# Kernel tuning notes

Measured on AMD Instinct MI355X. Metric: run time of the kernel, lower is better.

## Reference

```python
import jax, jax.numpy as jnp
import numpy as np

# ---- static config ----
B, D, H, W, C = 4, 8, 56, 56, 192
Md, Mh, Mw = 2, 7, 7
Sd, Sh, Sw = 1, 3, 3
NH = 6
HD = C // NH
SCALE = HD ** -0.5
N = Md * Mh * Mw  # 98
NW = (D // Md) * (H // Mh) * (W // Mw)  # 256 windows per batch element


def _rel_pos_index():
    coords = np.stack(np.meshgrid(np.arange(Md), np.arange(Mh), np.arange(Mw), indexing='ij'))
    cf = coords.reshape(3, -1)
    rc = (cf[:, :, None] - cf[:, None, :]).transpose(1, 2, 0)
    rc[..., 0] += Md - 1
    rc[..., 1] += Mh - 1
    rc[..., 2] += Mw - 1
    rc[..., 0] *= (2 * Mh - 1) * (2 * Mw - 1)
    rc[..., 1] *= 2 * Mw - 1
    return rc.sum(-1)  # (N, N) int

REL_IDX = jnp.asarray(_rel_pos_index())


def _build_attn_mask():
    img = np.zeros((D, H, W), dtype=np.float32)
    cnt = 0
    for ds in (slice(0, -Md), slice(-Md, -Sd), slice(-Sd, None)):
        for hs in (slice(0, -Mh), slice(-Mh, -Sh), slice(-Sh, None)):
            for ws in (slice(0, -Mw), slice(-Mw, -Sw), slice(-Sw, None)):
                img[ds, hs, ws] = cnt
                cnt += 1
    mw = img.reshape(D // Md, Md, H // Mh, Mh, W // Mw, Mw)
    mw = mw.transpose(0, 2, 4, 1, 3, 5).reshape(-1, N)  # (NW, N)
    am = mw[:, None, :] - mw[:, :, None]
    return np.where(am != 0, -100.0, 0.0).astype(np.float32)  # (NW, N, N)


def window_partition(x):  # (B, D, H, W, C) -> (B*NW, N, C)
    x = x.reshape(B, D // Md, Md, H // Mh, Mh, W // Mw, Mw, C)
    return x.transpose(0, 1, 3, 5, 2, 4, 6, 7).reshape(-1, N, C)


def window_reverse(w):  # (B*NW, N, C) -> (B, D, H, W, C)
    x = w.reshape(B, D // Md, H // Mh, W // Mw, Md, Mh, Mw, C)
    return x.transpose(0, 1, 4, 2, 5, 3, 6, 7).reshape(B, D, H, W, C)


def layer_norm(x, g, b, eps=1e-5):
    mu = x.mean(-1, keepdims=True)
    var = ((x - mu) ** 2).mean(-1, keepdims=True)
    return (x - mu) * jax.lax.rsqrt(var + eps) * g + b


def setup_inputs() -> dict:
    key = jax.random.key(0)
    ks = jax.random.split(key, 6)
    return {
        'x': jax.random.normal(ks[0], (B, D * H * W, C), jnp.float32),
        'attn_mask': jnp.asarray(_build_attn_mask()),
        'norm1_g': jnp.ones((C,), jnp.float32),
        'norm1_b': jnp.zeros((C,), jnp.float32),
        'qkv_w': jax.random.normal(ks[1], (3 * C, C), jnp.float32) * 0.02,
        'qkv_b': jnp.zeros((3 * C,), jnp.float32),
        'rel_bias': jax.random.normal(ks[2], ((2 * Md - 1) * (2 * Mh - 1) * (2 * Mw - 1), NH), jnp.float32) * 0.02,
        'proj_w': jax.random.normal(ks[3], (C, C), jnp.float32) * 0.02,
        'proj_b': jnp.zeros((C,), jnp.float32),
        'fc1_w': jax.random.normal(ks[4], (C, C), jnp.float32) * 0.02,
        'fc1_b': jnp.zeros((C,), jnp.float32),
    }


def reference(x, attn_mask, norm1_g, norm1_b, qkv_w, qkv_b, rel_bias, proj_w, proj_b, fc1_w, fc1_b):
    shortcut = x
    h = layer_norm(x, norm1_g, norm1_b).reshape(B, D, H, W, C)
    # cyclic shift (dims divisible by window -> no padding needed)
    h = jnp.roll(h, shift=(-Sd, -Sh, -Sw), axis=(1, 2, 3))
    xw = window_partition(h)  # (B*NW, N, C)
    B_ = xw.shape[0]
    qkv = (xw @ qkv_w.T + qkv_b).reshape(B_, N, 3, NH, HD).transpose(2, 0, 3, 1, 4)
    q, k, v = qkv[0], qkv[1], qkv[2]  # (B_, NH, N, HD)
    attn = jnp.einsum('bhnd,bhmd->bhnm', q * SCALE, k)
    bias = rel_bias[REL_IDX.reshape(-1)].reshape(N, N, NH).transpose(2, 0, 1)  # (NH, N, N)
    attn = attn + bias[None]
    # additive shift mask per window
    attn = attn.reshape(B, NW, NH, N, N) + attn_mask[None, :, None]
    attn = jax.nn.softmax(attn.reshape(B_, NH, N, N), axis=-1)
    out = jnp.einsum('bhnm,bhmd->bhnd', attn, v).transpose(0, 2, 1, 3).reshape(B_, N, C)
    out = out @ proj_w.T + proj_b
    h = window_reverse(out)
    h = jnp.roll(h, shift=(Sd, Sh, Sw), axis=(1, 2, 3)).reshape(B, D * H * W, C)
    h = jax.nn.gelu(h @ fc1_w.T + fc1_b, approximate=False)
    return shortcut + h
```

## Files before the change

### kernel.cpp

```cpp
#include <hip/hip_runtime.h>
#include <cstdint>
#include <cstddef>

typedef __bf16 bf16_t;
typedef __bf16 bf16x8 __attribute__((ext_vector_type(8)));
typedef float  f32x4  __attribute__((ext_vector_type(4)));

#define DHW   25088
#define SCALE 0.17677669529663687f

__device__ inline f32x4 mfma16(bf16x8 a, bf16x8 b, f32x4 c) {
  return __builtin_amdgcn_mfma_f32_16x16x32_bf16(a, b, c, 0, 0, 0);
}

__global__ __launch_bounds__(256) void prep_kernel(
    const float* __restrict__ qkv_w, const float* __restrict__ proj_w,
    const float* __restrict__ fc1_w,
    bf16_t* __restrict__ wq, bf16_t* __restrict__ wp, bf16_t* __restrict__ wf)
{
  int idx = blockIdx.x * 256 + threadIdx.x;
  if (idx < 110592) { wq[idx] = (bf16_t)qkv_w[idx]; return; }
  idx -= 110592;
  if (idx < 36864) { wp[idx] = (bf16_t)proj_w[idx]; return; }
  idx -= 36864;
  if (idx < 36864) { wf[idx] = (bf16_t)fc1_w[idx]; }
}

__global__ __launch_bounds__(256) void prep_bm_kernel(
    const float* __restrict__ rel_bias, const float* __restrict__ mask,
    bf16_t* __restrict__ bmr)
{
  int idx = blockIdx.x * 256 + threadIdx.x;
  int e    = idx & 31;
  int lane = (idx >> 5) & 63;
  int t    = idx >> 11;
  int mt   = t % 7;
  int wh   = t / 7;
  int winb = wh / 6, h = wh - winb * 6;
  int g = lane >> 4, li = lane & 15;
  int nt2 = e >> 2, v = e & 3;
  int row = mt * 16 + g * 4 + v;
  int col = nt2 * 16 + li;
  float val = -1e30f;
  if (row < 98 && col < 98 && nt2 < 7) {
    int di = row / 49 - col / 49 + 1;
    int hi = (row / 7) % 7 - (col / 7) % 7 + 6;
    int wi = row % 7 - col % 7 + 6;
    int rid = di * 169 + hi * 13 + wi;
    val = mask[winb * 9604 + row * 98 + col] + rel_bias[rid * 6 + h];
  }
  bmr[idx] = (bf16_t)val;
}

__global__ __launch_bounds__(256) void ln_kernel(
    const float* __restrict__ x, const float* __restrict__ gw,
    const float* __restrict__ bw_, bf16_t* __restrict__ xn)
{
  int orow = blockIdx.x * 4 + (threadIdx.x >> 6);
  int lane = threadIdx.x & 63;
  int win = orow / 98, tok = orow % 98;
  int b = win >> 8, wr = win & 255;
  int bd = wr >> 6, bh = (wr >> 3) & 7, bwi = wr & 7;
  int md = tok / 49, mh = (tok / 7) % 7, mw = tok % 7;
  int d = (bd * 2 + md + 1) & 7;
  int h = bh * 7 + mh + 3; if (h >= 56) h -= 56;
  int w = bwi * 7 + mw + 3; if (w >= 56) w -= 56;
  const float* xr = x + ((size_t)b * DHW + (size_t)((d * 56 + h) * 56 + w)) * 192;
  float v0 = xr[lane], v1 = xr[lane + 64], v2 = xr[lane + 128];
  float s = v0 + v1 + v2, sq = v0 * v0 + v1 * v1 + v2 * v2;
  #pragma unroll
  for (int off = 1; off < 64; off <<= 1) {
    s  += __shfl_xor(s,  off, 64);
    sq += __shfl_xor(sq, off, 64);
  }
  float mu = s * (1.0f / 192.0f);
  float var = sq * (1.0f / 192.0f) - mu * mu;
  float rstd = rsqrtf(var + 1e-5f);
  bf16_t* o = xn + (size_t)orow * 192;
  o[lane]       = (bf16_t)((v0 - mu) * rstd * gw[lane]       + bw_[lane]);
  o[lane + 64]  = (bf16_t)((v1 - mu) * rstd * gw[lane + 64]  + bw_[lane + 64]);
  o[lane + 128] = (bf16_t)((v2 - mu) * rstd * gw[lane + 128] + bw_[lane + 128]);
}

template<int MODE>
__global__ __launch_bounds__(256) void gemm_kernel(
    const bf16_t* __restrict__ A, const bf16_t* __restrict__ W,
    const float* __restrict__ bias, int ntiles, int ncols,
    bf16_t* __restrict__ outb, float* __restrict__ outf,
    const float* __restrict__ resid)
{
  __shared__ __align__(16) bf16_t As[64][200];
  __shared__ __align__(16) bf16_t Bs[64][200];
  int tid = threadIdx.x;
  int nt = blockIdx.x % ntiles, mt = blockIdx.x / ntiles;
  int row0 = mt * 64, n0 = nt * 64;
  #pragma unroll
  for (int i = 0; i < 6; i++) {
    int c = tid + 256 * i;
    int r = c / 24, ck = c % 24;
    *(uint4*)&As[r][ck * 8] = *(const uint4*)(A + (size_t)(row0 + r) * 192 + ck * 8);
    *(uint4*)&Bs[r][ck * 8] = *(const uint4*)(W + (size_t)(n0 + r) * 192 + ck * 8);
  }
  __syncthreads();
  int wid = tid >> 6, lane = tid & 63;
  int wm = wid >> 1, wn = wid & 1;
  int g = lane >> 4, li = lane & 15;
  f32x4 acc[2][2] = {};
  #pragma unroll
  for (int ks = 0; ks < 6; ks++) {
    int ko = ks * 32 + g * 8;
    bf16x8 a0 = *(const bf16x8*)&As[wm * 32 + li][ko];
    bf16x8 a1 = *(const bf16x8*)&As[wm * 32 + 16 + li][ko];
    bf16x8 b0 = *(const bf16x8*)&Bs[wn * 32 + li][ko];
    bf16x8 b1 = *(const bf16x8*)&Bs[wn * 32 + 16 + li][ko];
    acc[0][0] = mfma16(a0, b0, acc[0][0]);
    acc[0][1] = mfma16(a0, b1, acc[0][1]);
    acc[1][0] = mfma16(a1, b0, acc[1][0]);
    acc[1][1] = mfma16(a1, b1, acc[1][1]);
  }
  #pragma unroll
  for (int mi = 0; mi < 2; mi++)
  #pragma unroll
  for (int ni = 0; ni < 2; ni++)
  #pragma unroll
  for (int v = 0; v < 4; v++) {
    int row = row0 + wm * 32 + mi * 16 + g * 4 + v;
    int col = n0 + wn * 32 + ni * 16 + li;
    float val = acc[mi][ni][v] + bias[col];
    if (MODE == 0) {
      outb[(size_t)row * ncols + col] = (bf16_t)val;
    } else if (MODE == 1) {
      int win = row / 98, tok = row % 98;
      int b = win >> 8, wr = win & 255;
      int bd = wr >> 6, bh = (wr >> 3) & 7, bwi = wr & 7;
      int md = tok / 49, mh = (tok / 7) % 7, mw = tok % 7;
      int d = (bd * 2 + md + 1) & 7;
      int hh = bh * 7 + mh + 3; if (hh >= 56) hh -= 56;
      int w2 = bwi * 7 + mw + 3; if (w2 >= 56) w2 -= 56;
      size_t grow = (size_t)b * DHW + (size_t)((d * 56 + hh) * 56 + w2);
      outb[grow * 192 + col] = (bf16_t)val;
    } else {
      float ge = 0.5f * val * (1.0f + erff(val * 0.70710678118654752f));
      size_t o = (size_t)row * 192 + col;
      outf[o] = resid[o] + ge;
    }
  }
}

__global__ __launch_bounds__(448, 6) void attn_kernel(
    const bf16_t* __restrict__ qkv, const bf16_t* __restrict__ bmr,
    bf16_t* __restrict__ ao)
{
  __shared__ __align__(16) bf16_t U[15232];
  __shared__ __align__(16) bf16_t Vt[32][136];
  int bid = blockIdx.x;
  int h = bid % 6, win = bid / 6;
  int winb = win & 255;
  int tid = threadIdx.x;
  int wid = tid >> 6, lane = tid & 63;
  int mt = wid, g = lane >> 4, li = lane & 15;

  const bf16_t* bmp = bmr + ((((size_t)(winb * 6 + h)) * 7 + mt) * 64 + lane) * 32;
  bf16x8 bm0 = *(const bf16x8*)(bmp);
  bf16x8 bm1 = *(const bf16x8*)(bmp + 8);
  bf16x8 bm2 = *(const bf16x8*)(bmp + 16);
  bf16x8 bm3 = *(const bf16x8*)(bmp + 24);

  const bf16_t* base = qkv + (size_t)win * 98 * 576 + h * 32;
  #define QS(r, c) U[(r) * 40 + (c)]
  #define KS(r, c) U[4480 + (r) * 40 + (c)]
  #define PS(r, c) U[(r) * 136 + (c)]
  for (int c = tid; c < 784; c += 448) {
    int cc = c < 392 ? c : c - 392;
    int tok = cc >> 2, part = cc & 3;
    uint4 u = *(const uint4*)(base + (c < 392 ? 0 : 192) + tok * 576 + part * 8);
    if (c < 392) *(uint4*)&QS(tok, part * 8) = u;
    else         *(uint4*)&KS(tok, part * 8) = u;
  }
  if (tid < 112) {
    uint4 z = {0, 0, 0, 0};
    int a = tid >> 6;
    int r = 98 + ((tid & 63) >> 2), part = tid & 3;
    if (r < 112) {
      if (a == 0) *(uint4*)&QS(r, part * 8) = z;
      else        *(uint4*)&KS(r, part * 8) = z;
    }
  }
  if (tid < 392) {
    int tok = tid >> 2, part = tid & 3;
    bf16x8 u = *(const bf16x8*)(base + 384 + tok * 576 + part * 8);
    #pragma unroll
    for (int j = 0; j < 8; j++) Vt[part * 8 + j][tok] = u[j];
  }
  for (int e2 = tid; e2 < 960; e2 += 448) {
    int r = e2 / 30, ci = 98 + e2 % 30;
    Vt[r][ci] = (bf16_t)0.0f;
  }
  __syncthreads();

  bf16x8 af = *(const bf16x8*)&QS(mt * 16 + li, g * 8);
  float logit[7][4];
  #pragma unroll
  for (int nt2 = 0; nt2 < 7; nt2++) {
    bf16x8 bfr = *(const bf16x8*)&KS(nt2 * 16 + li, g * 8);
    f32x4 z = {};
    f32x4 S = mfma16(af, bfr, z);
    #pragma unroll
    for (int v = 0; v < 4; v++) {
      int e = nt2 * 4 + v;
      float bmv = (e < 8) ? (float)bm0[e] : (e < 16) ? (float)bm1[e - 8]
                : (e < 24) ? (float)bm2[e - 16] : (float)bm3[e - 24];
      logit[nt2][v] = S[v] * SCALE + bmv;
    }
  }
  __syncthreads();

  #pragma unroll
  for (int v = 0; v < 4; v++) {
    float mx = logit[0][v];
    #pragma unroll
    for (int nt2 = 1; nt2 < 7; nt2++) mx = fmaxf(mx, logit[nt2][v]);
    #pragma unroll
    for (int off = 1; off < 16; off <<= 1) mx = fmaxf(mx, __shfl_xor(mx, off, 64));
    float se = 0.f;
    #pragma unroll
    for (int nt2 = 0; nt2 < 7; nt2++) {
      float p = __expf(logit[nt2][v] - mx);
      logit[nt2][v] = p; se += p;
    }
    #pragma unroll
    for (int off = 1; off < 16; off <<= 1) se += __shfl_xor(se, off, 64);
    float inv = 1.0f / se;
    int row = mt * 16 + g * 4 + v;
    #pragma unroll
    for (int nt2 = 0; nt2 < 7; nt2++)
      PS(row, nt2 * 16 + li) = (bf16_t)(logit[nt2][v] * inv);
    PS(row, 112 + li) = (bf16_t)0.0f;
  }
  f32x4 o0 = {}, o1 = {};
  #pragma unroll
  for (int ks = 0; ks < 4; ks++) {
    int ko = ks * 32 + g * 8;
    bf16x8 pf = *(const bf16x8*)&PS(mt * 16 + li, ko);
    bf16x8 v0 = *(const bf16x8*)&Vt[li][ko];
    bf16x8 v1 = *(const bf16x8*)&Vt[16 + li][ko];
    o0 = mfma16(pf, v0, o0);
    o1 = mfma16(pf, v1, o1);
  }
  bf16_t* aout = ao + (size_t)win * 98 * 192 + h * 32;
  #pragma unroll
  for (int v = 0; v < 4; v++) {
    int row = mt * 16 + g * 4 + v;
    if (row < 98) {
      aout[(size_t)row * 192 + li]      = (bf16_t)o0[v];
      aout[(size_t)row * 192 + 16 + li] = (bf16_t)o1[v];
    }
  }
  #undef QS
  #undef KS
  #undef PS
}

extern "C" void kernel_launch(void* const* d_in, const int* in_sizes, int n_in,
                              void* d_out, int out_size, void* d_ws, size_t ws_size,
                              hipStream_t stream) {
  (void)in_sizes; (void)n_in; (void)out_size; (void)ws_size;
  const float* x         = (const float*)d_in[0];
  const float* attn_mask = (const float*)d_in[1];
  const float* n1g       = (const float*)d_in[2];
  const float* n1b       = (const float*)d_in[3];
  const float* qkv_w     = (const float*)d_in[4];
  const float* qkv_b     = (const float*)d_in[5];
  const float* rel_bias  = (const float*)d_in[6];
  const float* proj_w    = (const float*)d_in[7];
  const float* proj_b    = (const float*)d_in[8];
  const float* fc1_w     = (const float*)d_in[9];
  const float* fc1_b     = (const float*)d_in[10];
  float* out = (float*)d_out;

  char* ws = (char*)d_ws;
  size_t off = 0;
  auto alloc = [&](size_t bytes) -> char* {
    char* p = ws + off;
    off += (bytes + 255) & ~(size_t)255;
    return p;
  };
  bf16_t* wq  = (bf16_t*)alloc(110592 * 2);
  bf16_t* wp  = (bf16_t*)alloc(36864 * 2);
  bf16_t* wf  = (bf16_t*)alloc(36864 * 2);
  bf16_t* bmr = (bf16_t*)alloc((size_t)22020096 * 2);
  bf16_t* xn  = (bf16_t*)alloc((size_t)100352 * 192 * 2);
  bf16_t* qkv = (bf16_t*)alloc((size_t)100352 * 576 * 2);
  bf16_t* y   = (bf16_t*)alloc((size_t)100352 * 192 * 2);
  bf16_t* ao  = xn;

  prep_kernel<<<720, 256, 0, stream>>>(qkv_w, proj_w, fc1_w, wq, wp, wf);
  prep_bm_kernel<<<86016, 256, 0, stream>>>(rel_bias, attn_mask, bmr);
  ln_kernel<<<25088, 256, 0, stream>>>(x, n1g, n1b, xn);
  gemm_kernel<0><<<1568 * 9, 256, 0, stream>>>(xn, wq, qkv_b, 9, 576, qkv, nullptr, nullptr);
  attn_kernel<<<6144, 448, 0, stream>>>(qkv, bmr, ao);
  gemm_kernel<1><<<1568 * 3, 256, 0, stream>>>(ao, wp, proj_b, 3, 192, y, nullptr, nullptr);
  gemm_kernel<2><<<1568 * 3, 256, 0, stream>>>(y, wf, fc1_b, 3, 192, nullptr, out, x);
}
```

Before: 450.4 us.

## Fuse LayerNorm into QKV GEMM, fuse proj+fc1 GEMMs, dedupe mask-bias table

LayerNorm is folded into the QKV GEMM, which keeps a 64-row normalized A tile in registers and loops over all nine N tiles with register-prefetched weight tiles. The proj and fc1 GEMMs are merged into one kernel that keeps the projected tile in shared memory, so the intermediate y buffer never goes to global memory. The precomputed bias+mask table shrinks from 256 windows to 8 distinct window types, which cuts prep-kernel writes and attention-side reads. The cost is lower grid parallelism (1568 blocks) and heavier register use per block.

```diff
diff --git a/kernel.cpp b/kernel.cpp
--- a/kernel.cpp
+++ b/kernel.cpp
@@ -11,6 +11,17 @@
 
 __device__ inline f32x4 mfma16(bf16x8 a, bf16x8 b, f32x4 c) {
   return __builtin_amdgcn_mfma_f32_16x16x32_bf16(a, b, c, 0, 0, 0);
+}
+
+__device__ inline size_t wrow_to_grow(int orow) {
+  int win = orow / 98, tok = orow % 98;
+  int b = win >> 8, wr = win & 255;
+  int bd = wr >> 6, bh = (wr >> 3) & 7, bwi = wr & 7;
+  int md = tok / 49, mh = (tok / 7) % 7, mw = tok % 7;
+  int d = (bd * 2 + md + 1) & 7;
+  int h = bh * 7 + mh + 3; if (h >= 56) h -= 56;
+  int w = bwi * 7 + mw + 3; if (w >= 56) w -= 56;
+  return (size_t)b * DHW + (size_t)((d * 56 + h) * 56 + w);
 }
 
 __global__ __launch_bounds__(256) void prep_kernel(
@@ -33,10 +44,11 @@
   int idx = blockIdx.x * 256 + threadIdx.x;
   int e    = idx & 31;
   int lane = (idx >> 5) & 63;
-  int t    = idx >> 11;
-  int mt   = t % 7;
-  int wh   = t / 7;
-  int winb = wh / 6, h = wh - winb * 6;
+  int t2   = idx >> 11;
+  int mt   = t2 % 7;
+  int wh   = t2 / 7;
+  int type = wh / 6, h = wh - type * 6;
+  int winb = ((type & 4) ? 3 : 0) * 64 + ((type & 2) ? 7 : 0) * 8 + ((type & 1) ? 7 : 0);
   int g = lane >> 4, li = lane & 15;
   int nt2 = e >> 2, v = e & 3;
   int row = mt * 16 + g * 4 + v;
@@ -52,97 +64,98 @@
   bmr[idx] = (bf16_t)val;
 }
 
-__global__ __launch_bounds__(256) void ln_kernel(
+__global__ __launch_bounds__(256, 3) void lnqkv_kernel(
     const float* __restrict__ x, const float* __restrict__ gw,
-    const float* __restrict__ bw_, bf16_t* __restrict__ xn)
-{
-  int orow = blockIdx.x * 4 + (threadIdx.x >> 6);
-  int lane = threadIdx.x & 63;
-  int win = orow / 98, tok = orow % 98;
-  int b = win >> 8, wr = win & 255;
-  int bd = wr >> 6, bh = (wr >> 3) & 7, bwi = wr & 7;
-  int md = tok / 49, mh = (tok / 7) % 7, mw = tok % 7;
-  int d = (bd * 2 + md + 1) & 7;
-  int h = bh * 7 + mh + 3; if (h >= 56) h -= 56;
-  int w = bwi * 7 + mw + 3; if (w >= 56) w -= 56;
-  const float* xr = x + ((size_t)b * DHW + (size_t)((d * 56 + h) * 56 + w)) * 192;
-  float v0 = xr[lane], v1 = xr[lane + 64], v2 = xr[lane + 128];
-  float s = v0 + v1 + v2, sq = v0 * v0 + v1 * v1 + v2 * v2;
-  #pragma unroll
-  for (int off = 1; off < 64; off <<= 1) {
-    s  += __shfl_xor(s,  off, 64);
-    sq += __shfl_xor(sq, off, 64);
-  }
-  float mu = s * (1.0f / 192.0f);
-  float var = sq * (1.0f / 192.0f) - mu * mu;
-  float rstd = rsqrtf(var + 1e-5f);
-  bf16_t* o = xn + (size_t)orow * 192;
-  o[lane]       = (bf16_t)((v0 - mu) * rstd * gw[lane]       + bw_[lane]);
-  o[lane + 64]  = (bf16_t)((v1 - mu) * rstd * gw[lane + 64]  + bw_[lane + 64]);
-  o[lane + 128] = (bf16_t)((v2 - mu) * rstd * gw[lane + 128] + bw_[lane + 128]);
-}
-
-template<int MODE>
-__global__ __launch_bounds__(256) void gemm_kernel(
-    const bf16_t* __restrict__ A, const bf16_t* __restrict__ W,
-    const float* __restrict__ bias, int ntiles, int ncols,
-    bf16_t* __restrict__ outb, float* __restrict__ outf,
-    const float* __restrict__ resid)
+    const float* __restrict__ bw_, const bf16_t* __restrict__ wq,
+    const float* __restrict__ qkv_b, bf16_t* __restrict__ qkv)
 {
   __shared__ __align__(16) bf16_t As[64][200];
   __shared__ __align__(16) bf16_t Bs[64][200];
+  __shared__ float gws[192], bws[192], bias[576];
   int tid = threadIdx.x;
-  int nt = blockIdx.x % ntiles, mt = blockIdx.x / ntiles;
-  int row0 = mt * 64, n0 = nt * 64;
-  #pragma unroll
-  for (int i = 0; i < 6; i++) {
-    int c = tid + 256 * i;
-    int r = c / 24, ck = c % 24;
-    *(uint4*)&As[r][ck * 8] = *(const uint4*)(A + (size_t)(row0 + r) * 192 + ck * 8);
-    *(uint4*)&Bs[r][ck * 8] = *(const uint4*)(W + (size_t)(n0 + r) * 192 + ck * 8);
-  }
-  __syncthreads();
+  int row0 = blockIdx.x * 64;
+  if (tid < 192) { gws[tid] = gw[tid]; bws[tid] = bw_[tid]; }
+  for (int c = tid; c < 576; c += 256) bias[c] = qkv_b[c];
+
+  {
+    int r = tid >> 2, part = tid & 3;
+    size_t grow = wrow_to_grow(row0 + r);
+    const float* xr = x + grow * 192 + part * 48;
+    float v[48];
+    #pragma unroll
+    for (int i = 0; i < 12; i++) *(float4*)&v[i * 4] = *(const float4*)(xr + i * 4);
+    float s = 0.f, sq = 0.f;
+    #pragma unroll
+    for (int i = 0; i < 48; i++) { s += v[i]; sq += v[i] * v[i]; }
+    s += __shfl_xor(s, 1, 64); sq += __shfl_xor(sq, 1, 64);
+    s += __shfl_xor(s, 2, 64); sq += __shfl_xor(sq, 2, 64);
+    float mu = s * (1.0f / 192.0f);
+    float var = sq * (1.0f / 192.0f) - mu * mu;
+    float rstd = rsqrtf(var + 1e-5f);
+    __syncthreads();
+    bf16_t nb[48];
+    #pragma unroll
+    for (int i = 0; i < 48; i++) {
+      int c = part * 48 + i;
+      nb[i] = (bf16_t)((v[i] - mu) * rstd * gws[c] + bws[c]);
+    }
+    #pragma unroll
+    for (int j = 0; j < 6; j++)
+      *(bf16x8*)&As[r][part * 48 + j * 8] = *(bf16x8*)&nb[j * 8];
+  }
+  __syncthreads();
+
   int wid = tid >> 6, lane = tid & 63;
   int wm = wid >> 1, wn = wid & 1;
   int g = lane >> 4, li = lane & 15;
-  f32x4 acc[2][2] = {};
+  bf16x8 afr[2][6];
   #pragma unroll
   for (int ks = 0; ks < 6; ks++) {
-    int ko = ks * 32 + g * 8;
-    bf16x8 a0 = *(const bf16x8*)&As[wm * 32 + li][ko];
-    bf16x8 a1 = *(const bf16x8*)&As[wm * 32 + 16 + li][ko];
-    bf16x8 b0 = *(const bf16x8*)&Bs[wn * 32 + li][ko];
-    bf16x8 b1 = *(const bf16x8*)&Bs[wn * 32 + 16 + li][ko];
-    acc[0][0] = mfma16(a0, b0, acc[0][0]);
-    acc[0][1] = mfma16(a0, b1, acc[0][1]);
-    acc[1][0] = mfma16(a1, b0, acc[1][0]);
-    acc[1][1] = mfma16(a1, b1, acc[1][1]);
-  }
-  #pragma unroll
-  for (int mi = 0; mi < 2; mi++)
-  #pragma unroll
-  for (int ni = 0; ni < 2; ni++)
-  #pragma unroll
-  for (int v = 0; v < 4; v++) {
-    int row = row0 + wm * 32 + mi * 16 + g * 4 + v;
-    int col = n0 + wn * 32 + ni * 16 + li;
-    float val = acc[mi][ni][v] + bias[col];
-    if (MODE == 0) {
-      outb[(size_t)row * ncols + col] = (bf16_t)val;
-    } else if (MODE == 1) {
-      int win = row / 98, tok = row % 98;
-      int b = win >> 8, wr = win & 255;
-      int bd = wr >> 6, bh = (wr >> 3) & 7, bwi = wr & 7;
-      int md = tok / 49, mh = (tok / 7) % 7, mw = tok % 7;
-      int d = (bd * 2 + md + 1) & 7;
-      int hh = bh * 7 + mh + 3; if (hh >= 56) hh -= 56;
-      int w2 = bwi * 7 + mw + 3; if (w2 >= 56) w2 -= 56;
-      size_t grow = (size_t)b * DHW + (size_t)((d * 56 + hh) * 56 + w2);
-      outb[grow * 192 + col] = (bf16_t)val;
-    } else {
-      float ge = 0.5f * val * (1.0f + erff(val * 0.70710678118654752f));
-      size_t o = (size_t)row * 192 + col;
-      outf[o] = resid[o] + ge;
+    afr[0][ks] = *(const bf16x8*)&As[wm * 32 + li][ks * 32 + g * 8];
+    afr[1][ks] = *(const bf16x8*)&As[wm * 32 + 16 + li][ks * 32 + g * 8];
+  }
+
+  uint4 st[6];
+  #pragma unroll
+  for (int i = 0; i < 6; i++) {
+    int c = tid + 256 * i; int rr = c / 24, ck = c % 24;
+    st[i] = *(const uint4*)(wq + (size_t)rr * 192 + ck * 8);
+  }
+  for (int nt = 0; nt < 9; nt++) {
+    __syncthreads();
+    #pragma unroll
+    for (int i = 0; i < 6; i++) {
+      int c = tid + 256 * i; int rr = c / 24, ck = c % 24;
+      *(uint4*)&Bs[rr][ck * 8] = st[i];
+    }
+    __syncthreads();
+    if (nt < 8) {
+      #pragma unroll
+      for (int i = 0; i < 6; i++) {
+        int c = tid + 256 * i; int rr = c / 24, ck = c % 24;
+        st[i] = *(const uint4*)(wq + (size_t)(nt + 1) * 12288 + (size_t)rr * 192 + ck * 8);
+      }
+    }
+    f32x4 acc[2][2] = {};
+    #pragma unroll
+    for (int ks = 0; ks < 6; ks++) {
+      int ko = ks * 32 + g * 8;
+      bf16x8 b0 = *(const bf16x8*)&Bs[wn * 32 + li][ko];
+      bf16x8 b1 = *(const bf16x8*)&Bs[wn * 32 + 16 + li][ko];
+      acc[0][0] = mfma16(afr[0][ks], b0, acc[0][0]);
+      acc[0][1] = mfma16(afr[0][ks], b1, acc[0][1]);
+      acc[1][0] = mfma16(afr[1][ks], b0, acc[1][0]);
+      acc[1][1] = mfma16(afr[1][ks], b1, acc[1][1]);
+    }
+    #pragma unroll
+    for (int mi = 0; mi < 2; mi++)
+    #pragma unroll
+    for (int ni = 0; ni < 2; ni++)
+    #pragma unroll
+    for (int v = 0; v < 4; v++) {
+      int row = row0 + wm * 32 + mi * 16 + g * 4 + v;
+      int col = nt * 64 + wn * 32 + ni * 16 + li;
+      qkv[(size_t)row * 576 + col] = (bf16_t)(acc[mi][ni][v] + bias[col]);
     }
   }
 }
@@ -156,11 +169,13 @@
   int bid = blockIdx.x;
   int h = bid % 6, win = bid / 6;
   int winb = win & 255;
+  int type = (((winb >> 6) == 3) ? 4 : 0) | ((((winb >> 3) & 7) == 7) ? 2 : 0)
+           | (((winb & 7) == 7) ? 1 : 0);
   int tid = threadIdx.x;
   int wid = tid >> 6, lane = tid & 63;
   int mt = wid, g = lane >> 4, li = lane & 15;
 
-  const bf16_t* bmp = bmr + ((((size_t)(winb * 6 + h)) * 7 + mt) * 64 + lane) * 32;
+  const bf16_t* bmp = bmr + ((((size_t)(type * 6 + h)) * 7 + mt) * 64 + lane) * 32;
   bf16x8 bm0 = *(const bf16x8*)(bmp);
   bf16x8 bm1 = *(const bf16x8*)(bmp + 8);
   bf16x8 bm2 = *(const bf16x8*)(bmp + 16);
@@ -259,6 +274,136 @@
   #undef QS
   #undef KS
   #undef PS
+}
+
+__global__ __launch_bounds__(256, 3) void pf_kernel(
+    const bf16_t* __restrict__ ao, const bf16_t* __restrict__ wp,
+    const float* __restrict__ proj_b, const bf16_t* __restrict__ wf,
+    const float* __restrict__ fc1_b, const float* __restrict__ x,
+    float* __restrict__ out)
+{
+  __shared__ __align__(16) bf16_t As[64][200];
+  __shared__ __align__(16) bf16_t Bs[64][200];
+  __shared__ float pb[192], fb[192];
+  int tid = threadIdx.x;
+  int row0 = blockIdx.x * 64;
+  if (tid < 192) { pb[tid] = proj_b[tid]; fb[tid] = fc1_b[tid]; }
+  #pragma unroll
+  for (int i = 0; i < 6; i++) {
+    int c = tid + 256 * i; int rr = c / 24, ck = c % 24;
+    *(uint4*)&As[rr][ck * 8] = *(const uint4*)(ao + (size_t)(row0 + rr) * 192 + ck * 8);
+  }
+  __syncthreads();
+
+  int wid = tid >> 6, lane = tid & 63;
+  int wm = wid >> 1, wn = wid & 1;
+  int g = lane >> 4, li = lane & 15;
+  bf16x8 afr[2][6];
+  #pragma unroll
+  for (int ks = 0; ks < 6; ks++) {
+    afr[0][ks] = *(const bf16x8*)&As[wm * 32 + li][ks * 32 + g * 8];
+    afr[1][ks] = *(const bf16x8*)&As[wm * 32 + 16 + li][ks * 32 + g * 8];
+  }
+  __syncthreads();
+
+  uint4 st[6];
+  #pragma unroll
+  for (int i = 0; i < 6; i++) {
+    int c = tid + 256 * i; int rr = c / 24, ck = c % 24;
+    st[i] = *(const uint4*)(wp + (size_t)rr * 192 + ck * 8);
+  }
+  for (int nt = 0; nt < 3; nt++) {
+    __syncthreads();
+    #pragma unroll
+    for (int i = 0; i < 6; i++) {
+      int c = tid + 256 * i; int rr = c / 24, ck = c % 24;
+      *(uint4*)&Bs[rr][ck * 8] = st[i];
+    }
+    __syncthreads();
+    if (nt < 2) {
+      #pragma unroll
+      for (int i = 0; i < 6; i++) {
+        int c = tid + 256 * i; int rr = c / 24, ck = c % 24;
+        st[i] = *(const uint4*)(wp + (size_t)(nt + 1) * 12288 + (size_t)rr * 192 + ck * 8);
+      }
+    }
+    f32x4 acc[2][2] = {};
+    #pragma unroll
+    for (int ks = 0; ks < 6; ks++) {
+      int ko = ks * 32 + g * 8;
+      bf16x8 b0 = *(const bf16x8*)&Bs[wn * 32 + li][ko];
+      bf16x8 b1 = *(const bf16x8*)&Bs[wn * 32 + 16 + li][ko];
+      acc[0][0] = mfma16(afr[0][ks], b0, acc[0][0]);
+      acc[0][1] = mfma16(afr[0][ks], b1, acc[0][1]);
+      acc[1][0] = mfma16(afr[1][ks], b0, acc[1][0]);
+      acc[1][1] = mfma16(afr[1][ks], b1, acc[1][1]);
+    }
+    #pragma unroll
+    for (int mi = 0; mi < 2; mi++)
+    #pragma unroll
+    for (int ni = 0; ni < 2; ni++)
+    #pragma unroll
+    for (int v = 0; v < 4; v++) {
+      int rloc = wm * 32 + mi * 16 + g * 4 + v;
+      int col = nt * 64 + wn * 32 + ni * 16 + li;
+      As[rloc][col] = (bf16_t)(acc[mi][ni][v] + pb[col]);
+    }
+  }
+  __syncthreads();
+
+  bf16x8 a2[2][6];
+  #pragma unroll
+  for (int ks = 0; ks < 6; ks++) {
+    a2[0][ks] = *(const bf16x8*)&As[wm * 32 + li][ks * 32 + g * 8];
+    a2[1][ks] = *(const bf16x8*)&As[wm * 32 + 16 + li][ks * 32 + g * 8];
+  }
+  #pragma unroll
+  for (int i = 0; i < 6; i++) {
+    int c = tid + 256 * i; int rr = c / 24, ck = c % 24;
+    st[i] = *(const uint4*)(wf + (size_t)rr * 192 + ck * 8);
+  }
+  for (int nt = 0; nt < 3; nt++) {
+    __syncthreads();
+    #pragma unroll
+    for (int i = 0; i < 6; i++) {
+      int c = tid + 256 * i; int rr = c / 24, ck = c % 24;
+      *(uint4*)&Bs[rr][ck * 8] = st[i];
+    }
+    __syncthreads();
+    if (nt < 2) {
+      #pragma unroll
+      for (int i = 0; i < 6; i++) {
+        int c = tid + 256 * i; int rr = c / 24, ck = c % 24;
+        st[i] = *(const uint4*)(wf + (size_t)(nt + 1) * 12288 + (size_t)rr * 192 + ck * 8);
+      }
+    }
+    f32x4 acc[2][2] = {};
+    #pragma unroll
+    for (int ks = 0; ks < 6; ks++) {
+      int ko = ks * 32 + g * 8;
+      bf16x8 b0 = *(const bf16x8*)&Bs[wn * 32 + li][ko];
+      bf16x8 b1 = *(const bf16x8*)&Bs[wn * 32 + 16 + li][ko];
+      acc[0][0] = mfma16(a2[0][ks], b0, acc[0][0]);
+      acc[0][1] = mfma16(a2[0][ks], b1, acc[0][1]);
+      acc[1][0] = mfma16(a2[1][ks], b0, acc[1][0]);
+      acc[1][1] = mfma16(a2[1][ks], b1, acc[1][1]);
+    }
+    #pragma unroll
+    for (int mi = 0; mi < 2; mi++)
+    #pragma unroll
+    for (int v = 0; v < 4; v++) {
+      int rloc = wm * 32 + mi * 16 + g * 4 + v;
+      size_t grow = wrow_to_grow(row0 + rloc);
+      #pragma unroll
+      for (int ni = 0; ni < 2; ni++) {
+        int col = nt * 64 + wn * 32 + ni * 16 + li;
+        float val = acc[mi][ni][v] + fb[col];
+        float ge = 0.5f * val * (1.0f + erff(val * 0.70710678118654752f));
+        size_t o = grow * 192 + col;
+        out[o] = x[o] + ge;
+      }
+    }
+  }
 }
 
 extern "C" void kernel_launch(void* const* d_in, const int* in_sizes, int n_in,
@@ -288,17 +433,13 @@
   bf16_t* wq  = (bf16_t*)alloc(110592 * 2);
   bf16_t* wp  = (bf16_t*)alloc(36864 * 2);
   bf16_t* wf  = (bf16_t*)alloc(36864 * 2);
-  bf16_t* bmr = (bf16_t*)alloc((size_t)22020096 * 2);
-  bf16_t* xn  = (bf16_t*)alloc((size_t)100352 * 192 * 2);
+  bf16_t* bmr = (bf16_t*)alloc((size_t)688128 * 2);
   bf16_t* qkv = (bf16_t*)alloc((size_t)100352 * 576 * 2);
-  bf16_t* y   = (bf16_t*)alloc((size_t)100352 * 192 * 2);
-  bf16_t* ao  = xn;
+  bf16_t* ao  = (bf16_t*)alloc((size_t)100352 * 192 * 2);
 
   prep_kernel<<<720, 256, 0, stream>>>(qkv_w, proj_w, fc1_w, wq, wp, wf);
-  prep_bm_kernel<<<86016, 256, 0, stream>>>(rel_bias, attn_mask, bmr);
-  ln_kernel<<<25088, 256, 0, stream>>>(x, n1g, n1b, xn);
-  gemm_kernel<0><<<1568 * 9, 256, 0, stream>>>(xn, wq, qkv_b, 9, 576, qkv, nullptr, nullptr);
+  prep_bm_kernel<<<2688, 256, 0, stream>>>(rel_bias, attn_mask, bmr);
+  lnqkv_kernel<<<1568, 256, 0, stream>>>(x, n1g, n1b, wq, qkv_b, qkv);
   attn_kernel<<<6144, 448, 0, stream>>>(qkv, bmr, ao);
-  gemm_kernel<1><<<1568 * 3, 256, 0, stream>>>(ao, wp, proj_b, 3, 192, y, nullptr, nullptr);
-  gemm_kernel<2><<<1568 * 3, 256, 0, stream>>>(y, wf, fc1_b, 3, 192, nullptr, out, x);
-}
+  pf_kernel<<<1568, 256, 0, stream>>>(ao, wp, proj_b, wf, fc1_b, x, out);
+}
```

After: 423.9 us. 1.06x faster.
